# Kernel tuning notes

Measured on AMD Instinct MI355X. Metric: run time of the kernel, lower is better.

Reference implementation:

```python
import jax, jax.numpy as jnp
import numpy as np

B, S, E, H, DK, DV = 2, 2048, 1024, 16, 64, 64
NEG = -1e9


def setup_inputs() -> dict:
    key = jax.random.key(0)
    ks = jax.random.split(key, 12)
    s = 0.02
    return {
        "query": jax.random.normal(ks[0], (B, S, E), jnp.float32),
        "key": jax.random.normal(ks[1], (B, S, E), jnp.float32),
        "value": jax.random.normal(ks[2], (B, S, E), jnp.float32),
        "mask": jax.random.randint(ks[3], (B, S, S), 0, 2, jnp.int32),
        "Wq": jax.random.normal(ks[4], (E, H * DK), jnp.float32) * s,
        "bq": jnp.zeros((H * DK,), jnp.float32),
        "Wk": jax.random.normal(ks[5], (E, H * DK), jnp.float32) * s,
        "bk": jnp.zeros((H * DK,), jnp.float32),
        "Wv": jax.random.normal(ks[6], (E, H * DV), jnp.float32) * s,
        "bv": jnp.zeros((H * DV,), jnp.float32),
        "Wo": jax.random.normal(ks[7], (H * DV, E), jnp.float32) * s,
        "bo": jnp.zeros((E,), jnp.float32),
    }


def reference(query, key, value, mask, Wq, bq, Wk, bk, Wv, bv, Wo, bo):
    # projections, then split heads: (B,S,H*D) -> (B,H,S,D)
    q = (query @ Wq + bq).reshape(B, S, H, DK).transpose(0, 2, 1, 3)
    k = (key @ Wk + bk).reshape(B, S, H, DK).transpose(0, 2, 1, 3)
    v = (value @ Wv + bv).reshape(B, S, H, DV).transpose(0, 2, 1, 3)
    scores = jnp.einsum("bhqd,bhkd->bhqk", q, k) / jnp.sqrt(jnp.float32(DK))
    scores = jnp.where(mask[:, None, :, :] == 0, jnp.float32(NEG), scores)
    weights = jax.nn.softmax(scores, axis=-1)
    ctx = jnp.einsum("bhqk,bhkd->bhqd", weights, v)
    ctx = ctx.transpose(0, 2, 1, 3).reshape(B, S, H * DV)
    return ctx @ Wo + bo
```

## Files before the change

### kernel.cpp

```cpp
#include <hip/hip_runtime.h>

typedef __attribute__((ext_vector_type(8))) short s16x8;
typedef __attribute__((ext_vector_type(4))) float f32x4;
typedef __attribute__((ext_vector_type(16))) float f32x16;
typedef unsigned short u16;
typedef unsigned int u32;
typedef unsigned long long u64;

__device__ __forceinline__ u16 f2bf(float f) {
  u32 u = __builtin_bit_cast(u32, f);
  u += 0x7fff + ((u >> 16) & 1);
  return (u16)(u >> 16);
}

__device__ __forceinline__ float exp2fast(float x) {
#if __has_builtin(__builtin_amdgcn_exp2f)
  return __builtin_amdgcn_exp2f(x);
#else
  return __expf(x * 0.6931471805599453f);
#endif
}

__device__ __forceinline__ void gload16(const void* g, void* l) {
  __builtin_amdgcn_global_load_lds((const __attribute__((address_space(1))) u32*)g,
                                   (__attribute__((address_space(3))) u32*)l, 16, 0, 0);
}

#define MFMA(a, b, c) __builtin_amdgcn_mfma_f32_16x16x32_bf16((a), (b), (c), 0, 0, 0)
#define MFMA32(a, b, c) __builtin_amdgcn_mfma_f32_32x32x16_bf16((a), (b), (c), 0, 0, 0)

#define QSCALE 0.18033688011112042f

__global__ __launch_bounds__(256) void cvt_bf16_3(const float* __restrict__ q,
                                                  const float* __restrict__ k,
                                                  const float* __restrict__ v,
                                                  u16* __restrict__ oq, u16* __restrict__ ok,
                                                  u16* __restrict__ ov) {
  int z = blockIdx.y;
  const float* src = (z == 0) ? q : (z == 1) ? k : v;
  u16* dst = (z == 0) ? oq : (z == 1) ? ok : ov;
  int i = blockIdx.x * 256 + threadIdx.x;
  const float4* s4 = (const float4*)src;
  float4 a = s4[2 * i], b = s4[2 * i + 1];
  uint4 o;
  o.x = (u32)f2bf(a.x) | ((u32)f2bf(a.y) << 16);
  o.y = (u32)f2bf(a.z) | ((u32)f2bf(a.w) << 16);
  o.z = (u32)f2bf(b.x) | ((u32)f2bf(b.y) << 16);
  o.w = (u32)f2bf(b.z) | ((u32)f2bf(b.w) << 16);
  ((uint4*)dst)[i] = o;
}

__global__ __launch_bounds__(256) void mask_bits(const int* __restrict__ mask,
                                                 u64* __restrict__ mb) {
  int wi = (blockIdx.x * 256 + threadIdx.x) >> 6;
  int lane = threadIdx.x & 63;
  u64 bits = __ballot(mask[((size_t)wi << 6) + lane] != 0);
  if (lane == 0) mb[wi] = bits;
}

__global__ __launch_bounds__(256) void transpose_w4(const float* __restrict__ W0,
                                                    const float* __restrict__ W1,
                                                    const float* __restrict__ W2,
                                                    const float* __restrict__ W3,
                                                    u16* __restrict__ T0, u16* __restrict__ T1,
                                                    u16* __restrict__ T2, u16* __restrict__ T3) {
  int z = blockIdx.z;
  const float* W = (z == 0) ? W0 : (z == 1) ? W1 : (z == 2) ? W2 : W3;
  u16* WT = (z == 0) ? T0 : (z == 1) ? T1 : (z == 2) ? T2 : T3;
  __shared__ float t[32][33];
  int tx = threadIdx.x, ty = threadIdx.y;
  int n = blockIdx.x * 32 + tx;
#pragma unroll
  for (int j = 0; j < 4; j++) {
    int k = blockIdx.y * 32 + ty + 8 * j;
    t[ty + 8 * j][tx] = W[(size_t)k * 1024 + n];
  }
  __syncthreads();
  int k = blockIdx.y * 32 + tx;
#pragma unroll
  for (int j = 0; j < 4; j++) {
    int n2 = blockIdx.x * 32 + ty + 8 * j;
    WT[(size_t)n2 * 1024 + k] = f2bf(t[tx][ty + 8 * j]);
  }
}

template <int BM, int BN>
__device__ __forceinline__ void gemm_core(const u16* __restrict__ A, const u16* __restrict__ BT,
                                          int m0, int n0, u16* Ash, u16* Bsh,
                                          f32x4 (&acc)[BM / 32][BN / 32]) {
  constexpr int MF = BM / 32, NF = BN / 32;
  constexpr int BATCH = BM / 32 + BN / 32;
  const int tid = threadIdx.x;
  const int lane = tid & 63, wid = tid >> 6;
  const int r16 = lane & 15, g = lane >> 4;
  const int wm = wid >> 1, wn = wid & 1;
  const int swz = r16 & 7;
  const f32x4 vz = {0.f, 0.f, 0.f, 0.f};
#pragma unroll
  for (int mf = 0; mf < MF; mf++)
#pragma unroll
    for (int nf = 0; nf < NF; nf++) acc[mf][nf] = vz;

  auto stage = [&](int buf, int k0) {
#pragma unroll
    for (int i = 0; i < MF; i++) {
      int ch = i * 256 + tid;
      int row = ch >> 3, sc = (ch & 7) ^ (row & 7);
      gload16(A + (((size_t)(m0 + row)) << 10) + k0 + sc * 8,
              Ash + (size_t)buf * (BM * 64) + ch * 8);
    }
#pragma unroll
    for (int i = 0; i < NF; i++) {
      int ch = i * 256 + tid;
      int row = ch >> 3, sc = (ch & 7) ^ (row & 7);
      gload16(BT + (((size_t)(n0 + row)) << 10) + k0 + sc * 8,
              Bsh + (size_t)buf * (BN * 64) + ch * 8);
    }
  };

  asm volatile("" ::: "memory");
  stage(0, 0);
  asm volatile("" ::: "memory");
  stage(1, 64);
  asm volatile("" ::: "memory");

  for (int t = 0; t < 16; t++) {
    const int cur = t & 1;
    if (t == 15) {
      asm volatile("s_waitcnt vmcnt(0)" ::: "memory");
    } else if constexpr (BATCH == 8) {
      asm volatile("s_waitcnt vmcnt(8)" ::: "memory");
    } else {
      asm volatile("s_waitcnt vmcnt(6)" ::: "memory");
    }
    asm volatile("s_barrier" ::: "memory");

    const u16* Acur = Ash + (size_t)cur * (BM * 64);
    const u16* Bcur = Bsh + (size_t)cur * (BN * 64);
    __builtin_amdgcn_s_setprio(1);
#pragma unroll
    for (int kk = 0; kk < 2; kk++) {
      const int c = (kk * 4 + g);
      s16x8 af[MF], bfr[NF];
#pragma unroll
      for (int mf = 0; mf < MF; mf++)
        af[mf] = *(const s16x8*)(Acur + ((wm * (BM / 2) + mf * 16 + r16) << 6) +
                                 ((c ^ swz) << 3));
#pragma unroll
      for (int nf = 0; nf < NF; nf++)
        bfr[nf] = *(const s16x8*)(Bcur + ((wn * (BN / 2) + nf * 16 + r16) << 6) +
                                  ((c ^ swz) << 3));
#pragma unroll
      for (int mf = 0; mf < MF; mf++)
#pragma unroll
        for (int nf = 0; nf < NF; nf++) acc[mf][nf] = MFMA(af[mf], bfr[nf], acc[mf][nf]);
    }
    __builtin_amdgcn_s_setprio(0);

    asm volatile("s_barrier" ::: "memory");
    if (t + 2 < 16) stage(cur, (t + 2) * 64);
  }
}

__global__ __launch_bounds__(256, 2) void proj_gemm(
    const u16* __restrict__ Xq, const u16* __restrict__ Xk, const u16* __restrict__ Xv,
    const u16* __restrict__ WqT, const u16* __restrict__ WkT, const u16* __restrict__ WvT,
    const float* __restrict__ bq, const float* __restrict__ bk, const float* __restrict__ bv,
    u16* __restrict__ Qo, u16* __restrict__ Ko, u16* __restrict__ Vto) {
  __shared__ u16 Ash[2 * 128 * 64], Bsh[2 * 128 * 64];
  const int z = blockIdx.z;
  const u16* A = (z == 0) ? Xq : (z == 1) ? Xk : Xv;
  const u16* BT = (z == 0) ? WqT : (z == 1) ? WkT : WvT;
  const float* bias = (z == 0) ? bq : (z == 1) ? bk : bv;
  u16* O = (z == 0) ? Qo : (z == 1) ? Ko : Vto;
  const float sc = (z == 0) ? QSCALE : 1.0f;
  const int m0 = blockIdx.y * 128, n0 = blockIdx.x * 128;
  f32x4 acc[4][4];
  gemm_core<128, 128>(A, BT, m0, n0, Ash, Bsh, acc);
  const int tid = threadIdx.x, lane = tid & 63, wid = tid >> 6;
  const int r16 = lane & 15, g = lane >> 4, wm = wid >> 1, wn = wid & 1;
#pragma unroll
  for (int nf = 0; nf < 4; nf++) {
    int col = n0 + wn * 64 + nf * 16 + r16;
    float bb = bias[col];
    int h = col >> 6, d = col & 63;
#pragma unroll
    for (int mf = 0; mf < 4; mf++) {
#pragma unroll
      for (int ri = 0; ri < 4; ri++) {
        int row = m0 + wm * 64 + mf * 16 + g * 4 + ri;
        int b_ = row >> 11, s_ = row & 2047;
        u16 val = f2bf((acc[mf][nf][ri] + bb) * sc);
        if (z < 2)
          O[((((size_t)b_ * 16 + h) * 2048 + s_) << 6) + d] = val;
        else
          O[((((size_t)b_ * 16 + h) * 64 + d) << 11) + s_] = val;
      }
    }
  }
}

__global__ __launch_bounds__(256, 2) void out_gemm(const u16* __restrict__ ctx,
                                                   const u16* __restrict__ WoT,
                                                   const float* __restrict__ bo,
                                                   float* __restrict__ out) {
  __shared__ u16 Ash[2 * 64 * 64], Bsh[2 * 128 * 64];
  const int m0 = blockIdx.y * 64, n0 = blockIdx.x * 128;
  f32x4 acc[2][4];
  gemm_core<64, 128>(ctx, WoT, m0, n0, Ash, Bsh, acc);
  const int tid = threadIdx.x, lane = tid & 63, wid = tid >> 6;
  const int r16 = lane & 15, g = lane >> 4, wm = wid >> 1, wn = wid & 1;
#pragma unroll
  for (int nf = 0; nf < 4; nf++) {
    int col = n0 + wn * 64 + nf * 16 + r16;
    float bb = bo[col];
#pragma unroll
    for (int mf = 0; mf < 2; mf++) {
#pragma unroll
      for (int ri = 0; ri < 4; ri++) {
        int row = m0 + wm * 32 + mf * 16 + g * 4 + ri;
        out[((size_t)row << 10) + col] = acc[mf][nf][ri] + bb;
      }
    }
  }
}

__device__ __forceinline__ s16x8 pack4u(u32 a0, u32 a1, u32 b0, u32 b1) {
  union { u32 u[4]; s16x8 v; } p;
  p.u[0] = a0; p.u[1] = a1; p.u[2] = b0; p.u[3] = b1;
  return p.v;
}

__device__ __forceinline__ float bflo(u32 pk) { return __builtin_bit_cast(float, pk << 16); }
__device__ __forceinline__ float bfhi(u32 pk) { return __builtin_bit_cast(float, pk & 0xFFFF0000u); }

__device__ __forceinline__ void softpack(const f32x16& sv, u32 wm, s16x8& pA, s16x8& pB,
                                         float& rs) {
  float e[16];
#pragma unroll
  for (int qd = 0; qd < 4; qd++)
#pragma unroll
    for (int j = 0; j < 4; j++)
      e[qd * 4 + j] = exp2fast(sv[qd * 4 + j]) * (float)((wm >> (qd * 8 + j)) & 1);
#pragma unroll
  for (int n = 0; n < 2; n++) {
    u32 a0, a1, b0, b1;
    asm("v_cvt_pk_bf16_f32 %0, %1, %2" : "=v"(a0) : "v"(e[n * 8 + 0]), "v"(e[n * 8 + 1]));
    asm("v_cvt_pk_bf16_f32 %0, %1, %2" : "=v"(a1) : "v"(e[n * 8 + 2]), "v"(e[n * 8 + 3]));
    asm("v_cvt_pk_bf16_f32 %0, %1, %2" : "=v"(b0) : "v"(e[n * 8 + 4]), "v"(e[n * 8 + 5]));
    asm("v_cvt_pk_bf16_f32 %0, %1, %2" : "=v"(b1) : "v"(e[n * 8 + 6]), "v"(e[n * 8 + 7]));
    rs += ((bflo(a0) + bfhi(a0)) + (bflo(a1) + bfhi(a1))) +
          ((bflo(b0) + bfhi(b0)) + (bflo(b1) + bfhi(b1)));
    asm("v_permlane32_swap_b32 %0, %1" : "+v"(a0), "+v"(b0));
    asm("v_permlane32_swap_b32 %0, %1" : "+v"(a1), "+v"(b1));
    if (n == 0) pA = pack4u(a0, a1, b0, b1);
    else        pB = pack4u(a0, a1, b0, b1);
  }
}

__global__ __launch_bounds__(256, 2) void flash_attn(const u16* __restrict__ Q,
                                                     const u16* __restrict__ K,
                                                     const u16* __restrict__ Vt,
                                                     const u64* __restrict__ Mb64,
                                                     u16* __restrict__ ctx) {
  __shared__ __align__(16) u16 Ksh[4][64][64];
  __shared__ __align__(16) u16 Vsh[4][64][64];

  const int tid = threadIdx.x, w = tid >> 6, lane = tid & 63;
  const int l31 = lane & 31, h5 = lane >> 5, l7 = lane & 7;

  int work = ((int)blockIdx.x & 7) * 64 + ((int)blockIdx.x >> 3);
  const int qt = work & 15, bh = work >> 4;
  const int b = bh >> 4, h = bh & 15;
  const int q0 = qt * 128 + w * 32;

  const u16* Qb = Q + ((size_t)bh << 17);
  const u16* Kb = K + ((size_t)bh << 17);
  const u16* Vb = Vt + ((size_t)bh << 17);
  const u64* Mrow = Mb64 + ((size_t)(b * 2048 + q0 + l31) << 5);

  const int srow = tid >> 3, sk16 = tid & 7;
#define STAGE(buf, kv0)                                                                   \
  {                                                                                       \
    _Pragma("unroll") for (int i = 0; i < 2; i++) {                                       \
      int row = i * 32 + srow;                                                            \
      int sc = sk16 ^ (row & 7);                                                          \
      gload16(Kb + (((size_t)((kv0) + row)) << 6) + sc * 8,                               \
              (char*)&Ksh[buf][0][0] + (i * 256 + tid) * 16);                             \
      gload16(Vb + (((size_t)row) << 11) + (kv0) + sc * 8,                                \
              (char*)&Vsh[buf][0][0] + (i * 256 + tid) * 16);                             \
    }                                                                                     \
  }

  s16x8 aq[4];
#pragma unroll
  for (int dk = 0; dk < 4; dk++)
    aq[dk] = *(const s16x8*)(Qb + ((q0 + l31) << 6) + dk * 16 + h5 * 8);
  asm volatile("" ::: "memory");
  STAGE(0, 0);
  STAGE(1, 64);
  u64 m_c0 = Mrow[0], m_c1 = Mrow[1];
  asm volatile("" ::: "memory");
  STAGE(2, 128);
  STAGE(3, 192);
  u64 m_n0 = Mrow[2], m_n1 = Mrow[3];
  asm volatile("" ::: "memory");

  f32x16 o0, o1;
#pragma unroll
  for (int r = 0; r < 16; r++) { o0[r] = 0.f; o1[r] = 0.f; }
  float rs = 0.f;

  for (int t = 0; t < 16; t++) {
    const int base = (t & 1) * 2;
    if (t == 15) {
      asm volatile("s_waitcnt vmcnt(0)" ::: "memory");
    } else {
      asm volatile("s_waitcnt vmcnt(10)" ::: "memory");
    }
    asm volatile("s_barrier" ::: "memory");

    const u16* KcA = &Ksh[base][0][0];
    const u16* KcB = &Ksh[base + 1][0][0];
    const u16* VcA = &Vsh[base][0][0];
    const u16* VcB = &Vsh[base + 1][0][0];

    f32x16 s0, s1, s2, s3;
#pragma unroll
    for (int r = 0; r < 16; r++) { s0[r] = 0.f; s1[r] = 0.f; s2[r] = 0.f; s3[r] = 0.f; }
    __builtin_amdgcn_s_setprio(1);
#pragma unroll
    for (int dk = 0; dk < 4; dk++) {
      int ch = (((dk << 1) + h5) ^ l7) << 3;
      s16x8 akA0 = *(const s16x8*)(KcA + (l31 << 6) + ch);
      s16x8 akA1 = *(const s16x8*)(KcA + ((32 + l31) << 6) + ch);
      s16x8 akB0 = *(const s16x8*)(KcB + (l31 << 6) + ch);
      s16x8 akB1 = *(const s16x8*)(KcB + ((32 + l31) << 6) + ch);
      s0 = MFMA32(akA0, aq[dk], s0);
      s1 = MFMA32(akA1, aq[dk], s1);
      s2 = MFMA32(akB0, aq[dk], s2);
      s3 = MFMA32(akB1, aq[dk], s3);
    }
    __builtin_amdgcn_s_setprio(0);

    u64 mshA = m_c0 >> (h5 << 2);
    s16x8 pa[4];
    softpack(s0, (u32)mshA, pa[0], pa[1], rs);
    softpack(s1, (u32)(mshA >> 32), pa[2], pa[3], rs);
    __builtin_amdgcn_s_setprio(1);
#pragma unroll
    for (int km = 0; km < 4; km++) {
      int ch = (((km << 1) + h5) ^ l7) << 3;
      s16x8 bv0 = *(const s16x8*)(VcA + (l31 << 6) + ch);
      s16x8 bv1 = *(const s16x8*)(VcA + ((32 + l31) << 6) + ch);
      o0 = MFMA32(pa[km], bv0, o0);
      o1 = MFMA32(pa[km], bv1, o1);
    }
    __builtin_amdgcn_s_setprio(0);

    u64 mshB = m_c1 >> (h5 << 2);
    s16x8 pb[4];
    softpack(s2, (u32)mshB, pb[0], pb[1], rs);
    softpack(s3, (u32)(mshB >> 32), pb[2], pb[3], rs);
    __builtin_amdgcn_s_setprio(1);
#pragma unroll
    for (int km = 0; km < 4; km++) {
      int ch = (((km << 1) + h5) ^ l7) << 3;
      s16x8 bv0 = *(const s16x8*)(VcB + (l31 << 6) + ch);
      s16x8 bv1 = *(const s16x8*)(VcB + ((32 + l31) << 6) + ch);
      o0 = MFMA32(pb[km], bv0, o0);
      o1 = MFMA32(pb[km], bv1, o1);
    }
    __builtin_amdgcn_s_setprio(0);

    asm volatile("s_barrier" ::: "memory");
    u64 mw0 = 0, mw1 = 0;
    if (t + 2 < 16) {
      STAGE(base, (2 * t + 4) * 64);
      STAGE(base + 1, (2 * t + 5) * 64);
      mw0 = Mrow[2 * t + 4];
      mw1 = Mrow[2 * t + 5];
    }
    m_c0 = m_n0; m_c1 = m_n1;
    m_n0 = mw0;  m_n1 = mw1;
  }
#undef STAGE

  rs += __shfl_xor(rs, 32, 64);
  float inv = 1.f / rs;

#pragma unroll
  for (int r = 0; r < 16; r++) {
    int qr = (r & 3) + 8 * (r >> 2) + 4 * h5;
    float iv = __shfl(inv, qr, 64);
    size_t rowoff = ((size_t)((b << 11) + q0 + qr)) << 10;
    ctx[rowoff + (h << 6) + l31]      = f2bf(o0[r] * iv);
    ctx[rowoff + (h << 6) + 32 + l31] = f2bf(o1[r] * iv);
  }
}

extern "C" void kernel_launch(void* const* d_in, const int* in_sizes, int n_in,
                              void* d_out, int out_size, void* d_ws, size_t ws_size,
                              hipStream_t stream) {
  const float* query = (const float*)d_in[0];
  const float* key_  = (const float*)d_in[1];
  const float* value = (const float*)d_in[2];
  const int*   mask  = (const int*)d_in[3];
  const float* Wq = (const float*)d_in[4];
  const float* bq = (const float*)d_in[5];
  const float* Wk = (const float*)d_in[6];
  const float* bk = (const float*)d_in[7];
  const float* Wv = (const float*)d_in[8];
  const float* bv = (const float*)d_in[9];
  const float* Wo = (const float*)d_in[10];
  const float* bo = (const float*)d_in[11];

  const size_t MB = 1048576;
  char* ws = (char*)d_ws;
  u16* Xq  = (u16*)(ws + 0 * MB);
  u16* Xk  = (u16*)(ws + 8 * MB);
  u16* Xv  = (u16*)(ws + 16 * MB);
  u16* WqT = (u16*)(ws + 24 * MB);
  u16* WkT = (u16*)(ws + 26 * MB);
  u16* WvT = (u16*)(ws + 28 * MB);
  u16* WoT = (u16*)(ws + 30 * MB);
  u16* Qd  = (u16*)(ws + 32 * MB);
  u16* Kd  = (u16*)(ws + 40 * MB);
  u16* Vtd = (u16*)(ws + 48 * MB);
  u16* ctx = (u16*)(ws + 56 * MB);
  u64* Mb  = (u64*)(ws + 72 * MB);

  cvt_bf16_3<<<dim3(2048, 3), 256, 0, stream>>>(query, key_, value, Xq, Xk, Xv);
  mask_bits<<<32768, 256, 0, stream>>>(mask, Mb);

  dim3 tb(32, 8);
  transpose_w4<<<dim3(32, 32, 4), tb, 0, stream>>>(Wq, Wk, Wv, Wo, WqT, WkT, WvT, WoT);

  proj_gemm<<<dim3(8, 32, 3), 256, 0, stream>>>(Xq, Xk, Xv, WqT, WkT, WvT, bq, bk, bv,
                                                Qd, Kd, Vtd);
  flash_attn<<<512, 256, 0, stream>>>(Qd, Kd, Vtd, Mb, ctx);
  out_gemm<<<dim3(8, 64), 256, 0, stream>>>(ctx, WoT, bo, (float*)d_out);
}
```

Baseline: 157.9 us.

## Merge prep kernels into one launch and compute softmax row sums via MFMA

Combines the three preprocessing kernels (input bf16 conversion, weight transpose, mask bit packing) into a single kernel that picks its role from the block index, removing two launches. In attention, the row sum that used scalar unpack-and-add on every tile is now computed by an extra MFMA against a ones vector, so each lane already holds the denominator for its row and the final shuffles go away. The mask multiply becomes a sign-extended bitwise AND. Costs are more MFMA issue and an extra 16-register accumulator, which may add register pressure at the two-blocks-per-CU launch bound.

```diff
diff --git a/kernel.cpp b/kernel.cpp
--- a/kernel.cpp
+++ b/kernel.cpp
@@ -31,56 +31,53 @@
 
 #define QSCALE 0.18033688011112042f
 
-__global__ __launch_bounds__(256) void cvt_bf16_3(const float* __restrict__ q,
-                                                  const float* __restrict__ k,
-                                                  const float* __restrict__ v,
-                                                  u16* __restrict__ oq, u16* __restrict__ ok,
-                                                  u16* __restrict__ ov) {
-  int z = blockIdx.y;
-  const float* src = (z == 0) ? q : (z == 1) ? k : v;
-  u16* dst = (z == 0) ? oq : (z == 1) ? ok : ov;
-  int i = blockIdx.x * 256 + threadIdx.x;
-  const float4* s4 = (const float4*)src;
-  float4 a = s4[2 * i], b = s4[2 * i + 1];
-  uint4 o;
-  o.x = (u32)f2bf(a.x) | ((u32)f2bf(a.y) << 16);
-  o.y = (u32)f2bf(a.z) | ((u32)f2bf(a.w) << 16);
-  o.z = (u32)f2bf(b.x) | ((u32)f2bf(b.y) << 16);
-  o.w = (u32)f2bf(b.z) | ((u32)f2bf(b.w) << 16);
-  ((uint4*)dst)[i] = o;
-}
-
-__global__ __launch_bounds__(256) void mask_bits(const int* __restrict__ mask,
-                                                 u64* __restrict__ mb) {
-  int wi = (blockIdx.x * 256 + threadIdx.x) >> 6;
-  int lane = threadIdx.x & 63;
-  u64 bits = __ballot(mask[((size_t)wi << 6) + lane] != 0);
-  if (lane == 0) mb[wi] = bits;
-}
-
-__global__ __launch_bounds__(256) void transpose_w4(const float* __restrict__ W0,
-                                                    const float* __restrict__ W1,
-                                                    const float* __restrict__ W2,
-                                                    const float* __restrict__ W3,
-                                                    u16* __restrict__ T0, u16* __restrict__ T1,
-                                                    u16* __restrict__ T2, u16* __restrict__ T3) {
-  int z = blockIdx.z;
-  const float* W = (z == 0) ? W0 : (z == 1) ? W1 : (z == 2) ? W2 : W3;
-  u16* WT = (z == 0) ? T0 : (z == 1) ? T1 : (z == 2) ? T2 : T3;
+__global__ __launch_bounds__(256) void prep(
+    const float* __restrict__ q, const float* __restrict__ k, const float* __restrict__ v,
+    u16* __restrict__ oq, u16* __restrict__ ok, u16* __restrict__ ov,
+    const float* __restrict__ W0, const float* __restrict__ W1,
+    const float* __restrict__ W2, const float* __restrict__ W3,
+    u16* __restrict__ T0, u16* __restrict__ T1, u16* __restrict__ T2, u16* __restrict__ T3,
+    const int* __restrict__ mask, u64* __restrict__ mb) {
   __shared__ float t[32][33];
-  int tx = threadIdx.x, ty = threadIdx.y;
-  int n = blockIdx.x * 32 + tx;
-#pragma unroll
-  for (int j = 0; j < 4; j++) {
-    int k = blockIdx.y * 32 + ty + 8 * j;
-    t[ty + 8 * j][tx] = W[(size_t)k * 1024 + n];
-  }
-  __syncthreads();
-  int k = blockIdx.y * 32 + tx;
-#pragma unroll
-  for (int j = 0; j < 4; j++) {
-    int n2 = blockIdx.x * 32 + ty + 8 * j;
-    WT[(size_t)n2 * 1024 + k] = f2bf(t[tx][ty + 8 * j]);
+  const int bx = blockIdx.x, tid = threadIdx.x;
+  if (bx < 6144) {
+    int z = bx >> 11;
+    const float* src = (z == 0) ? q : (z == 1) ? k : v;
+    u16* dst = (z == 0) ? oq : (z == 1) ? ok : ov;
+    int i = (bx & 2047) * 256 + tid;
+    const float4* s4 = (const float4*)src;
+    float4 a = s4[2 * i], bb = s4[2 * i + 1];
+    uint4 o;
+    o.x = (u32)f2bf(a.x) | ((u32)f2bf(a.y) << 16);
+    o.y = (u32)f2bf(a.z) | ((u32)f2bf(a.w) << 16);
+    o.z = (u32)f2bf(bb.x) | ((u32)f2bf(bb.y) << 16);
+    o.w = (u32)f2bf(bb.z) | ((u32)f2bf(bb.w) << 16);
+    ((uint4*)dst)[i] = o;
+  } else if (bx < 10240) {
+    int r = bx - 6144;
+    int z = r >> 10, t2 = r & 1023;
+    const float* W = (z == 0) ? W0 : (z == 1) ? W1 : (z == 2) ? W2 : W3;
+    u16* WT = (z == 0) ? T0 : (z == 1) ? T1 : (z == 2) ? T2 : T3;
+    int nb = t2 & 31, kb = t2 >> 5;
+    int tx = tid & 31, ty = tid >> 5;
+    int n = nb * 32 + tx;
+#pragma unroll
+    for (int j = 0; j < 4; j++) {
+      int kk = kb * 32 + ty + 8 * j;
+      t[ty + 8 * j][tx] = W[(size_t)kk * 1024 + n];
+    }
+    __syncthreads();
+    int kk = kb * 32 + tx;
+#pragma unroll
+    for (int j = 0; j < 4; j++) {
+      int n2 = nb * 32 + ty + 8 * j;
+      WT[(size_t)n2 * 1024 + kk] = f2bf(t[tx][ty + 8 * j]);
+    }
+  } else {
+    int wi = (bx - 10240) * 4 + (tid >> 6);
+    int lane = tid & 63;
+    u64 bits = __ballot(mask[((size_t)wi << 6) + lane] != 0);
+    if (lane == 0) mb[wi] = bits;
   }
 }
 
@@ -231,17 +228,17 @@
   return p.v;
 }
 
-__device__ __forceinline__ float bflo(u32 pk) { return __builtin_bit_cast(float, pk << 16); }
-__device__ __forceinline__ float bfhi(u32 pk) { return __builtin_bit_cast(float, pk & 0xFFFF0000u); }
-
-__device__ __forceinline__ void softpack(const f32x16& sv, u32 wm, s16x8& pA, s16x8& pB,
-                                         float& rs) {
+__device__ __forceinline__ void softpack(const f32x16& sv, u32 wm, s16x8& pA, s16x8& pB) {
   float e[16];
 #pragma unroll
   for (int qd = 0; qd < 4; qd++)
 #pragma unroll
-    for (int j = 0; j < 4; j++)
-      e[qd * 4 + j] = exp2fast(sv[qd * 4 + j]) * (float)((wm >> (qd * 8 + j)) & 1);
+    for (int j = 0; j < 4; j++) {
+      const int bit = qd * 8 + j;
+      float ex = exp2fast(sv[qd * 4 + j]);
+      u32 sext = (u32)(((int)(wm << (31 - bit))) >> 31);
+      e[qd * 4 + j] = __builtin_bit_cast(float, __builtin_bit_cast(u32, ex) & sext);
+    }
 #pragma unroll
   for (int n = 0; n < 2; n++) {
     u32 a0, a1, b0, b1;
@@ -249,8 +246,6 @@
     asm("v_cvt_pk_bf16_f32 %0, %1, %2" : "=v"(a1) : "v"(e[n * 8 + 2]), "v"(e[n * 8 + 3]));
     asm("v_cvt_pk_bf16_f32 %0, %1, %2" : "=v"(b0) : "v"(e[n * 8 + 4]), "v"(e[n * 8 + 5]));
     asm("v_cvt_pk_bf16_f32 %0, %1, %2" : "=v"(b1) : "v"(e[n * 8 + 6]), "v"(e[n * 8 + 7]));
-    rs += ((bflo(a0) + bfhi(a0)) + (bflo(a1) + bfhi(a1))) +
-          ((bflo(b0) + bfhi(b0)) + (bflo(b1) + bfhi(b1)));
     asm("v_permlane32_swap_b32 %0, %1" : "+v"(a0), "+v"(b0));
     asm("v_permlane32_swap_b32 %0, %1" : "+v"(a1), "+v"(b1));
     if (n == 0) pA = pack4u(a0, a1, b0, b1);
@@ -306,10 +301,13 @@
   u64 m_n0 = Mrow[2], m_n1 = Mrow[3];
   asm volatile("" ::: "memory");
 
-  f32x16 o0, o1;
-#pragma unroll
-  for (int r = 0; r < 16; r++) { o0[r] = 0.f; o1[r] = 0.f; }
-  float rs = 0.f;
+  s16x8 vones;
+#pragma unroll
+  for (int j = 0; j < 8; j++) vones[j] = (short)0x3F80;
+
+  f32x16 o0, o1, o4;
+#pragma unroll
+  for (int r = 0; r < 16; r++) { o0[r] = 0.f; o1[r] = 0.f; o4[r] = 0.f; }
 
   for (int t = 0; t < 16; t++) {
     const int base = (t & 1) * 2;
@@ -345,8 +343,8 @@
 
     u64 mshA = m_c0 >> (h5 << 2);
     s16x8 pa[4];
-    softpack(s0, (u32)mshA, pa[0], pa[1], rs);
-    softpack(s1, (u32)(mshA >> 32), pa[2], pa[3], rs);
+    softpack(s0, (u32)mshA, pa[0], pa[1]);
+    softpack(s1, (u32)(mshA >> 32), pa[2], pa[3]);
     __builtin_amdgcn_s_setprio(1);
 #pragma unroll
     for (int km = 0; km < 4; km++) {
@@ -355,13 +353,14 @@
       s16x8 bv1 = *(const s16x8*)(VcA + ((32 + l31) << 6) + ch);
       o0 = MFMA32(pa[km], bv0, o0);
       o1 = MFMA32(pa[km], bv1, o1);
+      o4 = MFMA32(pa[km], vones, o4);
     }
     __builtin_amdgcn_s_setprio(0);
 
     u64 mshB = m_c1 >> (h5 << 2);
     s16x8 pb[4];
-    softpack(s2, (u32)mshB, pb[0], pb[1], rs);
-    softpack(s3, (u32)(mshB >> 32), pb[2], pb[3], rs);
+    softpack(s2, (u32)mshB, pb[0], pb[1]);
+    softpack(s3, (u32)(mshB >> 32), pb[2], pb[3]);
     __builtin_amdgcn_s_setprio(1);
 #pragma unroll
     for (int km = 0; km < 4; km++) {
@@ -370,6 +369,7 @@
       s16x8 bv1 = *(const s16x8*)(VcB + ((32 + l31) << 6) + ch);
       o0 = MFMA32(pb[km], bv0, o0);
       o1 = MFMA32(pb[km], bv1, o1);
+      o4 = MFMA32(pb[km], vones, o4);
     }
     __builtin_amdgcn_s_setprio(0);
 
@@ -386,14 +386,11 @@
   }
 #undef STAGE
 
-  rs += __shfl_xor(rs, 32, 64);
-  float inv = 1.f / rs;
-
 #pragma unroll
   for (int r = 0; r < 16; r++) {
     int qr = (r & 3) + 8 * (r >> 2) + 4 * h5;
-    float iv = __shfl(inv, qr, 64);
     size_t rowoff = ((size_t)((b << 11) + q0 + qr)) << 10;
+    float iv = 1.f / o4[r];
     ctx[rowoff + (h << 6) + l31]      = f2bf(o0[r] * iv);
     ctx[rowoff + (h << 6) + 32 + l31] = f2bf(o1[r] * iv);
   }
@@ -430,11 +427,8 @@
   u16* ctx = (u16*)(ws + 56 * MB);
   u64* Mb  = (u64*)(ws + 72 * MB);
 
-  cvt_bf16_3<<<dim3(2048, 3), 256, 0, stream>>>(query, key_, value, Xq, Xk, Xv);
-  mask_bits<<<32768, 256, 0, stream>>>(mask, Mb);
-
-  dim3 tb(32, 8);
-  transpose_w4<<<dim3(32, 32, 4), tb, 0, stream>>>(Wq, Wk, Wv, Wo, WqT, WkT, WvT, WoT);
+  prep<<<43008, 256, 0, stream>>>(query, key_, value, Xq, Xk, Xv,
+                                  Wq, Wk, Wv, Wo, WqT, WkT, WvT, WoT, mask, Mb);
 
   proj_gemm<<<dim3(8, 32, 3), 256, 0, stream>>>(Xq, Xk, Xv, WqT, WkT, WvT, bq, bk, bv,
                                                 Qd, Kd, Vtd);
```

After: 152.0 us. 1.04x faster.
